# Kernel optimization log

Hardware: AMD Instinct MI355X
Metric: run time of the kernel (lower is better)

## Reference

```python
import jax, jax.numpy as jnp
import numpy as np

EPS = 1e-5
K = 3
N_TAP = K * K


def _bn(x, g, b, m, v):
    # eval-mode batchnorm over channel axis 1 of NCHW
    inv = g / jnp.sqrt(v + EPS)
    return x * inv[None, :, None, None] + (b - m * inv)[None, :, None, None]


def _silu(x):
    return x * jax.nn.sigmoid(x)


def _dcn(x, offset, mask, w, b, pad=1):
    """Modulated deformable conv (DCNv2), stride 1.
    x: [B,C,H,W], offset: [B,2n,H,W] ((dy,dx) per tap), mask: [B,n,H,W],
    w: [O,C,K,K], b: [O]."""
    B, C, H, W = x.shape
    O = w.shape[0]
    ky, kx = jnp.meshgrid(jnp.arange(K), jnp.arange(K), indexing='ij')
    ky = ky.reshape(N_TAP).astype(x.dtype)
    kx = kx.reshape(N_TAP).astype(x.dtype)
    off = offset.reshape(B, N_TAP, 2, H, W)
    base_y = jnp.arange(H, dtype=x.dtype)[None, None, :, None]
    base_x = jnp.arange(W, dtype=x.dtype)[None, None, None, :]
    # fractional sample positions [B,n,H,W]
    py = base_y - pad + ky[None, :, None, None] + off[:, :, 0]
    px = base_x - pad + kx[None, :, None, None] + off[:, :, 1]
    y0 = jnp.floor(py)
    x0 = jnp.floor(px)
    fy = py - y0
    fx = px - x0
    y0i = y0.astype(jnp.int32)
    x0i = x0.astype(jnp.int32)
    x_flat = x.reshape(B, C, 1, H * W)

    def corner(yi, xi, wgt):
        valid = (yi >= 0) & (yi < H) & (xi >= 0) & (xi < W)
        idx = (jnp.clip(yi, 0, H - 1) * W + jnp.clip(xi, 0, W - 1)).reshape(B, 1, N_TAP, H * W)
        v = jnp.take_along_axis(x_flat, idx, axis=-1)  # [B,C,n,HW]
        return v * (wgt * valid.astype(x.dtype)).reshape(B, 1, N_TAP, H * W)

    acc = corner(y0i, x0i, (1 - fy) * (1 - fx))
    acc = acc + corner(y0i, x0i + 1, (1 - fy) * fx)
    acc = acc + corner(y0i + 1, x0i, fy * (1 - fx))
    acc = acc + corner(y0i + 1, x0i + 1, fy * fx)
    val = acc.reshape(B, C, N_TAP, H, W) * mask[:, None]  # modulation
    out = jnp.einsum('bcnhw,ocn->bohw', val, w.reshape(O, C, N_TAP))
    return out + b[None, :, None, None]


def setup_inputs() -> dict:
    key = jax.random.key(0)
    ks = jax.random.split(key, 16)
    B, C1, H, W = 8, 256, 80, 80
    C2 = 256
    Ch = 128  # c_ = int(c2 * 0.5)
    d = {}
    d['x'] = jax.random.normal(ks[0], (B, C1, H, W), jnp.float32)
    # cv1: 1x1 conv (no bias) + BN
    d['cv1_w'] = jax.random.normal(ks[1], (Ch, C1), jnp.float32) * (1.0 / np.sqrt(C1))
    d['bn1_g'] = jax.random.uniform(ks[2], (Ch,), jnp.float32, 0.5, 1.5)
    d['bn1_b'] = jax.random.normal(ks[3], (Ch,), jnp.float32) * 0.1
    d['bn1_m'] = jax.random.normal(ks[4], (Ch,), jnp.float32) * 0.1
    d['bn1_v'] = jax.random.uniform(ks[5], (Ch,), jnp.float32, 0.5, 1.5)
    # offset/mask predictor 3x3 conv (small weights -> modest deformation)
    d['off_w'] = jax.random.normal(ks[6], (3 * N_TAP, Ch, K, K), jnp.float32) * 0.01
    d['off_b'] = jnp.zeros((3 * N_TAP,), jnp.float32)
    # dcn main weight/bias
    d['dcn_w'] = jax.random.normal(ks[7], (Ch, Ch, K, K), jnp.float32) * (1.0 / np.sqrt(Ch * N_TAP))
    d['dcn_b'] = jnp.zeros((Ch,), jnp.float32)
    d['bn2_g'] = jax.random.uniform(ks[8], (Ch,), jnp.float32, 0.5, 1.5)
    d['bn2_b'] = jax.random.normal(ks[9], (Ch,), jnp.float32) * 0.1
    d['bn2_m'] = jax.random.normal(ks[10], (Ch,), jnp.float32) * 0.1
    d['bn2_v'] = jax.random.uniform(ks[11], (Ch,), jnp.float32, 0.5, 1.5)
    # cv2: 1x1 conv (no bias) + BN
    d['cv2_w'] = jax.random.normal(ks[12], (C2, Ch), jnp.float32) * (1.0 / np.sqrt(Ch))
    d['bn3_g'] = jax.random.uniform(ks[13], (C2,), jnp.float32, 0.5, 1.5)
    d['bn3_b'] = jax.random.normal(ks[14], (C2,), jnp.float32) * 0.1
    d['bn3_m'] = jax.random.normal(ks[15], (C2,), jnp.float32) * 0.1
    d['bn3_v'] = jnp.ones((C2,), jnp.float32)
    return d


def reference(x, cv1_w, bn1_g, bn1_b, bn1_m, bn1_v,
              off_w, off_b, dcn_w, dcn_b, bn2_g, bn2_b, bn2_m, bn2_v,
              cv2_w, bn3_g, bn3_b, bn3_m, bn3_v):
    # cv1: 1x1 conv -> BN -> SiLU
    y = _silu(_bn(jnp.einsum('bchw,oc->bohw', x, cv1_w), bn1_g, bn1_b, bn1_m, bn1_v))
    # offset/mask predictor: 3x3 conv, pad 1
    raw = jax.lax.conv_general_dilated(
        y, off_w, window_strides=(1, 1), padding=((1, 1), (1, 1)),
        dimension_numbers=('NCHW', 'OIHW', 'NCHW')) + off_b[None, :, None, None]
    offset = raw[:, :2 * N_TAP]
    mask = jax.nn.sigmoid(raw[:, 2 * N_TAP:])
    # modulated deformable 3x3 conv -> BN -> SiLU
    y = _silu(_bn(_dcn(y, offset, mask, dcn_w, dcn_b), bn2_g, bn2_b, bn2_m, bn2_v))
    # cv2: 1x1 conv -> BN -> SiLU
    y = _silu(_bn(jnp.einsum('bchw,oc->bohw', y, cv2_w), bn3_g, bn3_b, bn3_m, bn3_v))
    return x + y  # shortcut (c1 == c2)
```

## Files before the change

kernel.cpp:

```cpp
#include <hip/hip_runtime.h>
#include <math.h>

#define HWSZ 6400
#define WIMG 80
#define HIMG 80
#define BEPS 1e-5f

typedef __attribute__((ext_vector_type(8))) short short8;
typedef __attribute__((ext_vector_type(4))) float f32x4;
typedef __attribute__((ext_vector_type(4))) unsigned u32x4;

__device__ __forceinline__ unsigned short f2b(float f) {
    unsigned u = __builtin_bit_cast(unsigned, f);
    u += 0x7fffu + ((u >> 16) & 1u);
    return (unsigned short)(u >> 16);
}
__device__ __forceinline__ float silu_f(float t) { return t / (1.f + __expf(-t)); }

#define BMFMA(a, b, c) __builtin_amdgcn_mfma_f32_16x16x32_bf16(a, b, c, 0, 0, 0)

__global__ __launch_bounds__(256) void k_prep(
    const float* __restrict__ cv1w, const float* __restrict__ g1, const float* __restrict__ b1,
    const float* __restrict__ m1, const float* __restrict__ v1,
    const float* __restrict__ offw, const float* __restrict__ offb,
    const float* __restrict__ dcnw, const float* __restrict__ dcnb,
    const float* __restrict__ g2, const float* __restrict__ b2,
    const float* __restrict__ m2, const float* __restrict__ v2,
    const float* __restrict__ cv2w, const float* __restrict__ g3, const float* __restrict__ b3,
    const float* __restrict__ m3, const float* __restrict__ v3,
    unsigned short* __restrict__ apk1, unsigned short* __restrict__ apko,
    unsigned short* __restrict__ apkd, unsigned short* __restrict__ apk2,
    float* __restrict__ bias1, float* __restrict__ biaso,
    float* __restrict__ bias2, float* __restrict__ bias3)
{
    int idx = blockIdx.x * 256 + threadIdx.x;
    if (idx < 32768) {
        int j = idx & 7, L = (idx >> 3) & 63, ks = (idx >> 9) & 7, mt = idx >> 12;
        int o = mt * 16 + (L & 15), k = ks * 32 + (L >> 4) * 8 + j;
        float inv = g1[o] * rsqrtf(v1[o] + BEPS);
        apk1[idx] = f2b(cv1w[o * 256 + k] * inv);
    } else if (idx < 69632) {
        int t = idx - 32768;
        int j = t & 7, L = (t >> 3) & 63;
        int mt = t / 18432, rem = t % 18432, ks = rem >> 9;
        int o = mt * 16 + (L & 15);
        int kp = ks * 32 + (L >> 4) * 8 + j;
        int n = kp >> 7, c = kp & 127;
        float wv = (o < 27) ? offw[(size_t)(o * 128 + c) * 9 + n] : 0.f;
        apko[((size_t)(ks * 2 + mt) * 64 + L) * 8 + j] = f2b(wv);
    } else if (idx < 217088) {
        int t = idx - 69632;
        int j = t & 7, L = (t >> 3) & 63;
        int mt = t / 18432, rem = t % 18432, ks = rem >> 9;
        int o = mt * 16 + (L & 15);
        int kp = ks * 32 + (L >> 4) * 8 + j;
        int n = kp >> 7, c = kp & 127;
        float inv = g2[o] * rsqrtf(v2[o] + BEPS);
        apkd[((size_t)(ks * 8 + mt) * 64 + L) * 8 + j] = f2b(dcnw[(size_t)(o * 128 + c) * 9 + n] * inv);
    } else if (idx < 249856) {
        int t = idx - 217088;
        int j = t & 7, L = (t >> 3) & 63, ks = (t >> 9) & 3, mt = t >> 11;
        int o = mt * 16 + (L & 15), k = ks * 32 + (L >> 4) * 8 + j;
        float inv = g3[o] * rsqrtf(v3[o] + BEPS);
        apk2[((size_t)(ks * 16 + mt) * 64 + L) * 8 + j] = f2b(cv2w[o * 128 + k] * inv);
    } else if (idx < 250395) {
        int t = idx - 249856;
        if (t < 128) { float inv = g1[t] * rsqrtf(v1[t] + BEPS); bias1[t] = b1[t] - m1[t] * inv; }
        else if (t < 155) { biaso[t - 128] = offb[t - 128]; }
        else if (t < 283) { int o = t - 155; float inv = g2[o] * rsqrtf(v2[o] + BEPS);
                            bias2[o] = dcnb[o] * inv + b2[o] - m2[o] * inv; }
        else { int o = t - 283; float inv = g3[o] * rsqrtf(v3[o] + BEPS); bias3[o] = b3[o] - m3[o] * inv; }
    }
}

__global__ __launch_bounds__(256) void k_cv1(
    const float* __restrict__ x, const unsigned short* __restrict__ apk1,
    const float* __restrict__ bias1, unsigned short* __restrict__ y1t)
{
    __shared__ __align__(16) unsigned short sB[20480];
    int blk = blockIdx.x;
    int b = blk / 100, pt = blk % 100;
    int p0 = pt * 64;
    int tid = threadIdx.x;
    int lane = tid & 63;
    int w = tid >> 6;
    {
        int px = lane, q = w;
        const float* xb = x + (size_t)b * 256 * HWSZ + p0 + px;
        for (int ks = 0; ks < 8; ++ks) {
            unsigned pk[4];
#pragma unroll
            for (int t = 0; t < 4; ++t) {
                float f0 = xb[(size_t)(ks * 32 + q * 8 + 2 * t) * HWSZ];
                float f1 = xb[(size_t)(ks * 32 + q * 8 + 2 * t + 1) * HWSZ];
                asm("v_cvt_pk_bf16_f32 %0, %1, %2" : "=v"(pk[t]) : "v"(f0), "v"(f1));
            }
            *(u32x4*)&sB[((ks * 4 + (px >> 4)) * 16 + (px & 15)) * 40 + q * 8] =
                (u32x4){pk[0], pk[1], pk[2], pk[3]};
        }
    }
    __syncthreads();
    int n16 = lane & 15, qd = lane >> 4;
    f32x4 acc[2][4];
#pragma unroll
    for (int mi = 0; mi < 2; ++mi)
#pragma unroll
        for (int nt = 0; nt < 4; ++nt) acc[mi][nt] = (f32x4){0.f, 0.f, 0.f, 0.f};
    for (int ks = 0; ks < 8; ++ks) {
        short8 bf[4];
#pragma unroll
        for (int nt = 0; nt < 4; ++nt)
            bf[nt] = *(const short8*)&sB[((ks * 4 + nt) * 16 + n16) * 40 + qd * 8];
        short8 a0 = *(const short8*)&apk1[(size_t)(((w * 2 + 0) * 8 + ks) * 64 + lane) * 8];
        short8 a1 = *(const short8*)&apk1[(size_t)(((w * 2 + 1) * 8 + ks) * 64 + lane) * 8];
#pragma unroll
        for (int nt = 0; nt < 4; ++nt) acc[0][nt] = BMFMA(a0, bf[nt], acc[0][nt]);
#pragma unroll
        for (int nt = 0; nt < 4; ++nt) acc[1][nt] = BMFMA(a1, bf[nt], acc[1][nt]);
    }
    __syncthreads();
#pragma unroll
    for (int mi = 0; mi < 2; ++mi)
#pragma unroll
        for (int nt = 0; nt < 4; ++nt)
#pragma unroll
            for (int r = 0; r < 4; ++r) {
                int o = w * 32 + mi * 16 + qd * 4 + r;
                float sv = silu_f(acc[mi][nt][r] + bias1[o]);
                sB[(nt * 16 + n16) * 136 + o] = f2b(sv);
            }
    __syncthreads();
    {
        int px = tid >> 2, qq = tid & 3;
        unsigned short* ytb = y1t + ((size_t)b * HWSZ + p0 + px) * 128;
#pragma unroll
        for (int seg = 0; seg < 4; ++seg) {
            short8 v = *(const short8*)&sB[px * 136 + qq * 32 + seg * 8];
            *(short8*)&ytb[qq * 32 + seg * 8] = v;
        }
    }
}

#define HY2 8
#define HX2 20
#define NH 160

#define ACC8(uu, cb)                                                                   \
    {                                                                                  \
        _Pragma("unroll") for (int t = 0; t < 4; ++t) {                                \
            unsigned uv = (uu)[t];                                                     \
            av[(cb) + 2 * t] = fmaf(wk, __builtin_bit_cast(float, uv << 16),           \
                                    av[(cb) + 2 * t]);                                 \
            av[(cb) + 2 * t + 1] = fmaf(wk, __builtin_bit_cast(float, uv & 0xffff0000u),\
                                        av[(cb) + 2 * t + 1]);                         \
        }                                                                              \
    }

#define LDA8(dst, ksv)                                                                 \
    _Pragma("unroll") for (int mt_ = 0; mt_ < 8; ++mt_)                                \
        dst[mt_] = *(const short8*)&apkd[((size_t)((ksv) * 8 + mt_) * 64 + lane) * 8];

#define MF8(afX, bfv)                                                                  \
    _Pragma("unroll") for (int mt_ = 0; mt_ < 8; ++mt_)                                \
        acc[mt_] = BMFMA(afX[mt_], bfv, acc[mt_]);

#define PACKBF(bfv, sv)                                                                \
    short8 bfv;                                                                        \
    {                                                                                  \
        unsigned pk0, pk1, pk2, pk3;                                                   \
        asm("v_cvt_pk_bf16_f32 %0, %1, %2" : "=v"(pk0) : "v"(av[(sv)*8+0]), "v"(av[(sv)*8+1])); \
        asm("v_cvt_pk_bf16_f32 %0, %1, %2" : "=v"(pk1) : "v"(av[(sv)*8+2]), "v"(av[(sv)*8+3])); \
        asm("v_cvt_pk_bf16_f32 %0, %1, %2" : "=v"(pk2) : "v"(av[(sv)*8+4]), "v"(av[(sv)*8+5])); \
        asm("v_cvt_pk_bf16_f32 %0, %1, %2" : "=v"(pk3) : "v"(av[(sv)*8+6]), "v"(av[(sv)*8+7])); \
        bfv = __builtin_bit_cast(short8, (u32x4){pk0, pk1, pk2, pk3});                 \
    }

__global__ __launch_bounds__(256, 3) void k_odc(
    const unsigned short* __restrict__ y1t,
    const unsigned short* __restrict__ apko, const float* __restrict__ biaso,
    const unsigned short* __restrict__ apkd, const float* __restrict__ bias2,
    const unsigned short* __restrict__ apk2, const float* __restrict__ bias3,
    const float* __restrict__ x, float* __restrict__ out)
{
    __shared__ __align__(16) unsigned short sH[NH * 128];
    __shared__ float sRaw[27 * 66];

    int blk = blockIdx.x;
    int b = blk / 100, pt = blk % 100;
    int h0 = (pt / 5) * 4, w0 = (pt % 5) * 16;
    int tid = threadIdx.x, lane = tid & 63, w = tid >> 6;
    int n16 = lane & 15, qd = lane >> 4;
    int pxl = w * 16 + n16;
    const unsigned short* yb = y1t + (size_t)b * HWSZ * 128;

    for (int i = tid; i < NH * 16; i += 256) {
        int r = i >> 4, u = i & 15;
        int ly = r / HX2, lx = r % HX2;
        int yy = min(max(h0 + ly - 2, 0), HIMG - 1);
        int xx = min(max(w0 + lx - 2, 0), WIMG - 1);
        *(u32x4*)&sH[r * 128 + ((u ^ (r & 7)) * 8)] =
            *(const u32x4*)&yb[(size_t)(yy * WIMG + xx) * 128 + u * 8];
    }
    __syncthreads();

    {
        f32x4 oa0 = (f32x4){0.f, 0.f, 0.f, 0.f};
        f32x4 oa1 = (f32x4){0.f, 0.f, 0.f, 0.f};
        for (int n = 0; n < 9; ++n) {
            int dh = n / 3 - 1, dw = n % 3 - 1;
            int hh = h0 + w + dh, ww = w0 + n16 + dw;
            bool valid = ((unsigned)hh < HIMG) && ((unsigned)ww < WIMG);
            int r = (w + 2 + dh) * HX2 + (n16 + 2 + dw);
            int xr = r & 7;
            const unsigned short* hb = &sH[r * 128];
#pragma unroll
            for (int s = 0; s < 4; ++s) {
                short8 bf = *(const short8*)&hb[((s * 4 + qd) ^ xr) * 8];
                if (!valid) bf = (short8){0, 0, 0, 0, 0, 0, 0, 0};
                int ks = n * 4 + s;
                short8 a0 = *(const short8*)&apko[((size_t)(ks * 2 + 0) * 64 + lane) * 8];
                short8 a1 = *(const short8*)&apko[((size_t)(ks * 2 + 1) * 64 + lane) * 8];
                oa0 = BMFMA(a0, bf, oa0);
                oa1 = BMFMA(a1, bf, oa1);
            }
        }
#pragma unroll
        for (int mi = 0; mi < 2; ++mi)
#pragma unroll
            for (int r4 = 0; r4 < 4; ++r4) {
                int o = mi * 16 + qd * 4 + r4;
                if (o < 27) {
                    float t = (mi ? oa1[r4] : oa0[r4]) + biaso[o];
                    if (o >= 18) t = 1.f / (1.f + __expf(-t));
                    sRaw[o * 66 + pxl] = t;
                }
            }
    }
    __syncthreads();

    f32x4 acc[8];
#pragma unroll
    for (int mt = 0; mt < 8; ++mt) acc[mt] = (f32x4){0.f, 0.f, 0.f, 0.f};
    int hI = h0 + w, wI = w0 + n16;

    for (int n = 0; n < 9; ++n) {
        float dy = sRaw[(2 * n) * 66 + pxl];
        float dx = sRaw[(2 * n + 1) * 66 + pxl];
        float mk = sRaw[(18 + n) * 66 + pxl];
        float py = (float)(hI - 1 + n / 3) + dy;
        float px = (float)(wI - 1 + n % 3) + dx;
        float y0f = floorf(py), x0f = floorf(px);
        float fy = py - y0f, fxv = px - x0f;
        int y0 = (int)y0f, x0 = (int)x0f;
        float wy0 = (1.f - fy) * mk, wy1 = fy * mk, fx1 = 1.f - fxv;

        int ks0 = n * 4;
        short8 afA[8], afB[8];
        LDA8(afA, ks0)

        float av[32];
#pragma unroll
        for (int j = 0; j < 32; ++j) av[j] = 0.f;
#pragma unroll
        for (int k = 0; k < 4; ++k) {
            int yy = y0 + (k >> 1), xx = x0 + (k & 1);
            bool vld = ((unsigned)yy < HIMG) && ((unsigned)xx < WIMG);
            float wk = ((k >> 1) ? wy1 : wy0) * ((k & 1) ? fxv : fx1);
            if (!vld) wk = 0.f;
            int yc = min(max(yy, 0), HIMG - 1);
            int xc = min(max(xx, 0), WIMG - 1);
            int ly = yc - h0 + 2, lx = xc - w0 + 2;
            if (((unsigned)ly < HY2) && ((unsigned)lx < HX2)) {
                int r = ly * HX2 + lx;
                const unsigned short* hb = &sH[r * 128];
                int xr = r & 7;
                u32x4 u0 = *(const u32x4*)&hb[((0 + qd) ^ xr) * 8];
                u32x4 u1 = *(const u32x4*)&hb[((4 + qd) ^ xr) * 8];
                u32x4 u2 = *(const u32x4*)&hb[((8 + qd) ^ xr) * 8];
                u32x4 u3 = *(const u32x4*)&hb[((12 + qd) ^ xr) * 8];
                ACC8(u0, 0) ACC8(u1, 8) ACC8(u2, 16) ACC8(u3, 24)
            } else if (wk != 0.f) {
                const unsigned short* src = &yb[(size_t)(yc * WIMG + xc) * 128 + qd * 8];
                u32x4 u0 = *(const u32x4*)src;
                u32x4 u1 = *(const u32x4*)(src + 32);
                u32x4 u2 = *(const u32x4*)(src + 64);
                u32x4 u3 = *(const u32x4*)(src + 96);
                ACC8(u0, 0) ACC8(u1, 8) ACC8(u2, 16) ACC8(u3, 24)
            }
        }
        LDA8(afB, ks0 + 1)
        { PACKBF(bf0, 0) MF8(afA, bf0) }
        LDA8(afA, ks0 + 2)
        { PACKBF(bf1, 1) MF8(afB, bf1) }
        LDA8(afB, ks0 + 3)
        { PACKBF(bf2, 2) MF8(afA, bf2) }
        { PACKBF(bf3, 3) MF8(afB, bf3) }
    }
    __syncthreads();

    unsigned short* sE = sH;
#pragma unroll
    for (int mt = 0; mt < 8; ++mt)
#pragma unroll
        for (int r4 = 0; r4 < 4; ++r4) {
            int o = mt * 16 + qd * 4 + r4;
            float sv = silu_f(acc[mt][r4] + bias2[o]);
            sE[pxl * 136 + o] = f2b(sv);
        }
    __syncthreads();

    f32x4 c2[16];
#pragma unroll
    for (int mt = 0; mt < 16; ++mt) c2[mt] = (f32x4){0.f, 0.f, 0.f, 0.f};
#pragma unroll
    for (int ks = 0; ks < 4; ++ks) {
        short8 bf = *(const short8*)&sE[pxl * 136 + ks * 32 + qd * 8];
        short8 cfA[8], cfB[8];
#pragma unroll
        for (int mt_ = 0; mt_ < 8; ++mt_)
            cfA[mt_] = *(const short8*)&apk2[((size_t)(ks * 16 + mt_) * 64 + lane) * 8];
#pragma unroll
        for (int mt_ = 0; mt_ < 8; ++mt_)
            cfB[mt_] = *(const short8*)&apk2[((size_t)(ks * 16 + 8 + mt_) * 64 + lane) * 8];
#pragma unroll
        for (int mt_ = 0; mt_ < 8; ++mt_) c2[mt_] = BMFMA(cfA[mt_], bf, c2[mt_]);
#pragma unroll
        for (int mt_ = 0; mt_ < 8; ++mt_) c2[8 + mt_] = BMFMA(cfB[mt_], bf, c2[8 + mt_]);
    }
    int p = (h0 + w) * WIMG + w0 + n16;
    const float* xb = x + (size_t)b * 256 * HWSZ;
    float* ob = out + (size_t)b * 256 * HWSZ;
#pragma unroll
    for (int mt = 0; mt < 16; ++mt)
#pragma unroll
        for (int r4 = 0; r4 < 4; ++r4) {
            int o = mt * 16 + qd * 4 + r4;
            size_t idx = (size_t)o * HWSZ + p;
            ob[idx] = xb[idx] + silu_f(c2[mt][r4] + bias3[o]);
        }
}

extern "C" void kernel_launch(void* const* d_in, const int* in_sizes, int n_in,
                              void* d_out, int out_size, void* d_ws, size_t ws_size,
                              hipStream_t stream) {
    const float* x     = (const float*)d_in[0];
    const float* cv1w  = (const float*)d_in[1];
    const float* bn1g  = (const float*)d_in[2];
    const float* bn1b  = (const float*)d_in[3];
    const float* bn1m  = (const float*)d_in[4];
    const float* bn1v  = (const float*)d_in[5];
    const float* offw  = (const float*)d_in[6];
    const float* offb  = (const float*)d_in[7];
    const float* dcnw  = (const float*)d_in[8];
    const float* dcnb  = (const float*)d_in[9];
    const float* bn2g  = (const float*)d_in[10];
    const float* bn2b  = (const float*)d_in[11];
    const float* bn2m  = (const float*)d_in[12];
    const float* bn2v  = (const float*)d_in[13];
    const float* cv2w  = (const float*)d_in[14];
    const float* bn3g  = (const float*)d_in[15];
    const float* bn3b  = (const float*)d_in[16];
    const float* bn3m  = (const float*)d_in[17];
    const float* bn3v  = (const float*)d_in[18];
    float* out = (float*)d_out;

    float* base = (float*)d_ws;
    unsigned short* y1t = (unsigned short*)base;
    unsigned short* apk1 = (unsigned short*)(base + 7936000);
    unsigned short* apko = (unsigned short*)(base + 7952384);
    unsigned short* apkd = (unsigned short*)(base + 7970816);
    unsigned short* apk2 = (unsigned short*)(base + 8044544);
    float* bias1 = base + 8060928;
    float* biaso = base + 8061056;
    float* bias2 = base + 8061088;
    float* bias3 = base + 8061216;

    k_prep<<<979, 256, 0, stream>>>(cv1w, bn1g, bn1b, bn1m, bn1v,
                                    offw, offb, dcnw, dcnb,
                                    bn2g, bn2b, bn2m, bn2v,
                                    cv2w, bn3g, bn3b, bn3m, bn3v,
                                    apk1, apko, apkd, apk2,
                                    bias1, biaso, bias2, bias3);
    k_cv1<<<800, 256, 0, stream>>>(x, apk1, bias1, y1t);
    k_odc<<<800, 256, 0, stream>>>(y1t, apko, biaso, apkd, bias2,
                                   apk2, bias3, x, out);
}
```

Before: 245.5 us.

## Stage packed weight slabs into double-buffered LDS via async global_load_lds

Weight fragments for the offset conv, the deformable conv and cv2 were each read from global memory straight into registers by every wave. They are now split into 53 slabs of 8 KB, copied into a two-buffer LDS area with global_load_lds one slab ahead, and read back from LDS for the MFMAs. Each slab step adds a block-wide barrier, launch bounds drop from 3 to 2 blocks per CU, and LDS use grows by 16 KB. The goal is to hide weight-load latency and cut duplicated global and L2 traffic across waves, at the cost of lower occupancy and many more barriers.

```diff
diff --git a/kernel.cpp b/kernel.cpp
--- a/kernel.cpp
+++ b/kernel.cpp
@@ -18,6 +18,12 @@
 __device__ __forceinline__ float silu_f(float t) { return t / (1.f + __expf(-t)); }
 
 #define BMFMA(a, b, c) __builtin_amdgcn_mfma_f32_16x16x32_bf16(a, b, c, 0, 0, 0)
+
+__device__ __forceinline__ void gload16(const unsigned short* g, unsigned short* l) {
+    __builtin_amdgcn_global_load_lds(
+        (const __attribute__((address_space(1))) unsigned int*)g,
+        (__attribute__((address_space(3))) unsigned int*)l, 16, 0, 0);
+}
 
 __global__ __launch_bounds__(256) void k_prep(
     const float* __restrict__ cv1w, const float* __restrict__ g1, const float* __restrict__ b1,
@@ -144,6 +150,7 @@
 #define HY2 8
 #define HX2 20
 #define NH 160
+#define NSLAB 53
 
 #define ACC8(uu, cb)                                                                   \
     {                                                                                  \
@@ -156,26 +163,22 @@
         }                                                                              \
     }
 
-#define LDA8(dst, ksv)                                                                 \
-    _Pragma("unroll") for (int mt_ = 0; mt_ < 8; ++mt_)                                \
-        dst[mt_] = *(const short8*)&apkd[((size_t)((ksv) * 8 + mt_) * 64 + lane) * 8];
-
-#define MF8(afX, bfv)                                                                  \
-    _Pragma("unroll") for (int mt_ = 0; mt_ < 8; ++mt_)                                \
-        acc[mt_] = BMFMA(afX[mt_], bfv, acc[mt_]);
-
-#define PACKBF(bfv, sv)                                                                \
-    short8 bfv;                                                                        \
+__device__ __forceinline__ const unsigned short* slab_src(
+    const unsigned short* apko, const unsigned short* apkd,
+    const unsigned short* apk2, int i) {
+    if (i < 9)  return apko + (size_t)i * 4096;
+    if (i < 45) return apkd + (size_t)(i - 9) * 4096;
+    return apk2 + (size_t)(i - 45) * 4096;
+}
+
+#define STAGE(i, bp)                                                                   \
     {                                                                                  \
-        unsigned pk0, pk1, pk2, pk3;                                                   \
-        asm("v_cvt_pk_bf16_f32 %0, %1, %2" : "=v"(pk0) : "v"(av[(sv)*8+0]), "v"(av[(sv)*8+1])); \
-        asm("v_cvt_pk_bf16_f32 %0, %1, %2" : "=v"(pk1) : "v"(av[(sv)*8+2]), "v"(av[(sv)*8+3])); \
-        asm("v_cvt_pk_bf16_f32 %0, %1, %2" : "=v"(pk2) : "v"(av[(sv)*8+4]), "v"(av[(sv)*8+5])); \
-        asm("v_cvt_pk_bf16_f32 %0, %1, %2" : "=v"(pk3) : "v"(av[(sv)*8+6]), "v"(av[(sv)*8+7])); \
-        bfv = __builtin_bit_cast(short8, (u32x4){pk0, pk1, pk2, pk3});                 \
-    }
-
-__global__ __launch_bounds__(256, 3) void k_odc(
+        const unsigned short* src_ = slab_src(apko, apkd, apk2, (i));                  \
+        gload16(src_ + ((w * 2 + 0) * 512 + lane * 8), &sAf[bp][(w * 2 + 0) * 512]);   \
+        gload16(src_ + ((w * 2 + 1) * 512 + lane * 8), &sAf[bp][(w * 2 + 1) * 512]);   \
+    }
+
+__global__ __launch_bounds__(256, 2) void k_odc(
     const unsigned short* __restrict__ y1t,
     const unsigned short* __restrict__ apko, const float* __restrict__ biaso,
     const unsigned short* __restrict__ apkd, const float* __restrict__ bias2,
@@ -184,6 +187,7 @@
 {
     __shared__ __align__(16) unsigned short sH[NH * 128];
     __shared__ float sRaw[27 * 66];
+    __shared__ __align__(16) unsigned short sAf[2][4096];
 
     int blk = blockIdx.x;
     int b = blk / 100, pt = blk % 100;
@@ -201,12 +205,15 @@
         *(u32x4*)&sH[r * 128 + ((u ^ (r & 7)) * 8)] =
             *(const u32x4*)&yb[(size_t)(yy * WIMG + xx) * 128 + u * 8];
     }
+    STAGE(0, 0)
     __syncthreads();
+    int bufp = 0;
 
     {
         f32x4 oa0 = (f32x4){0.f, 0.f, 0.f, 0.f};
         f32x4 oa1 = (f32x4){0.f, 0.f, 0.f, 0.f};
         for (int n = 0; n < 9; ++n) {
+            STAGE(n + 1, bufp ^ 1)
             int dh = n / 3 - 1, dw = n % 3 - 1;
             int hh = h0 + w + dh, ww = w0 + n16 + dw;
             bool valid = ((unsigned)hh < HIMG) && ((unsigned)ww < WIMG);
@@ -217,26 +224,28 @@
             for (int s = 0; s < 4; ++s) {
                 short8 bf = *(const short8*)&hb[((s * 4 + qd) ^ xr) * 8];
                 if (!valid) bf = (short8){0, 0, 0, 0, 0, 0, 0, 0};
-                int ks = n * 4 + s;
-                short8 a0 = *(const short8*)&apko[((size_t)(ks * 2 + 0) * 64 + lane) * 8];
-                short8 a1 = *(const short8*)&apko[((size_t)(ks * 2 + 1) * 64 + lane) * 8];
+                short8 a0 = *(const short8*)&sAf[bufp][(s * 2 + 0) * 512 + lane * 8];
+                short8 a1 = *(const short8*)&sAf[bufp][(s * 2 + 1) * 512 + lane * 8];
                 oa0 = BMFMA(a0, bf, oa0);
                 oa1 = BMFMA(a1, bf, oa1);
             }
-        }
-#pragma unroll
-        for (int mi = 0; mi < 2; ++mi)
-#pragma unroll
-            for (int r4 = 0; r4 < 4; ++r4) {
-                int o = mi * 16 + qd * 4 + r4;
-                if (o < 27) {
-                    float t = (mi ? oa1[r4] : oa0[r4]) + biaso[o];
-                    if (o >= 18) t = 1.f / (1.f + __expf(-t));
-                    sRaw[o * 66 + pxl] = t;
-                }
-            }
-    }
-    __syncthreads();
+            if (n == 8) {
+#pragma unroll
+                for (int mi = 0; mi < 2; ++mi)
+#pragma unroll
+                    for (int r4 = 0; r4 < 4; ++r4) {
+                        int o = mi * 16 + qd * 4 + r4;
+                        if (o < 27) {
+                            float t = (mi ? oa1[r4] : oa0[r4]) + biaso[o];
+                            if (o >= 18) t = 1.f / (1.f + __expf(-t));
+                            sRaw[o * 66 + pxl] = t;
+                        }
+                    }
+            }
+            __syncthreads();
+            bufp ^= 1;
+        }
+    }
 
     f32x4 acc[8];
 #pragma unroll
@@ -244,88 +253,95 @@
     int hI = h0 + w, wI = w0 + n16;
 
     for (int n = 0; n < 9; ++n) {
-        float dy = sRaw[(2 * n) * 66 + pxl];
-        float dx = sRaw[(2 * n + 1) * 66 + pxl];
-        float mk = sRaw[(18 + n) * 66 + pxl];
-        float py = (float)(hI - 1 + n / 3) + dy;
-        float px = (float)(wI - 1 + n % 3) + dx;
-        float y0f = floorf(py), x0f = floorf(px);
-        float fy = py - y0f, fxv = px - x0f;
-        int y0 = (int)y0f, x0 = (int)x0f;
-        float wy0 = (1.f - fy) * mk, wy1 = fy * mk, fx1 = 1.f - fxv;
-
-        int ks0 = n * 4;
-        short8 afA[8], afB[8];
-        LDA8(afA, ks0)
-
         float av[32];
 #pragma unroll
-        for (int j = 0; j < 32; ++j) av[j] = 0.f;
-#pragma unroll
-        for (int k = 0; k < 4; ++k) {
-            int yy = y0 + (k >> 1), xx = x0 + (k & 1);
-            bool vld = ((unsigned)yy < HIMG) && ((unsigned)xx < WIMG);
-            float wk = ((k >> 1) ? wy1 : wy0) * ((k & 1) ? fxv : fx1);
-            if (!vld) wk = 0.f;
-            int yc = min(max(yy, 0), HIMG - 1);
-            int xc = min(max(xx, 0), WIMG - 1);
-            int ly = yc - h0 + 2, lx = xc - w0 + 2;
-            if (((unsigned)ly < HY2) && ((unsigned)lx < HX2)) {
-                int r = ly * HX2 + lx;
-                const unsigned short* hb = &sH[r * 128];
-                int xr = r & 7;
-                u32x4 u0 = *(const u32x4*)&hb[((0 + qd) ^ xr) * 8];
-                u32x4 u1 = *(const u32x4*)&hb[((4 + qd) ^ xr) * 8];
-                u32x4 u2 = *(const u32x4*)&hb[((8 + qd) ^ xr) * 8];
-                u32x4 u3 = *(const u32x4*)&hb[((12 + qd) ^ xr) * 8];
-                ACC8(u0, 0) ACC8(u1, 8) ACC8(u2, 16) ACC8(u3, 24)
-            } else if (wk != 0.f) {
-                const unsigned short* src = &yb[(size_t)(yc * WIMG + xc) * 128 + qd * 8];
-                u32x4 u0 = *(const u32x4*)src;
-                u32x4 u1 = *(const u32x4*)(src + 32);
-                u32x4 u2 = *(const u32x4*)(src + 64);
-                u32x4 u3 = *(const u32x4*)(src + 96);
-                ACC8(u0, 0) ACC8(u1, 8) ACC8(u2, 16) ACC8(u3, 24)
-            }
-        }
-        LDA8(afB, ks0 + 1)
-        { PACKBF(bf0, 0) MF8(afA, bf0) }
-        LDA8(afA, ks0 + 2)
-        { PACKBF(bf1, 1) MF8(afB, bf1) }
-        LDA8(afB, ks0 + 3)
-        { PACKBF(bf2, 2) MF8(afA, bf2) }
-        { PACKBF(bf3, 3) MF8(afB, bf3) }
-    }
-    __syncthreads();
-
-    unsigned short* sE = sH;
-#pragma unroll
-    for (int mt = 0; mt < 8; ++mt)
-#pragma unroll
-        for (int r4 = 0; r4 < 4; ++r4) {
-            int o = mt * 16 + qd * 4 + r4;
-            float sv = silu_f(acc[mt][r4] + bias2[o]);
-            sE[pxl * 136 + o] = f2b(sv);
-        }
-    __syncthreads();
-
+        for (int s = 0; s < 4; ++s) {
+            int slab = 9 + n * 4 + s;
+            if (slab + 1 < NSLAB) STAGE(slab + 1, bufp ^ 1)
+            if (s == 0) {
+                float dy = sRaw[(2 * n) * 66 + pxl];
+                float dx = sRaw[(2 * n + 1) * 66 + pxl];
+                float mk = sRaw[(18 + n) * 66 + pxl];
+                float py = (float)(hI - 1 + n / 3) + dy;
+                float px = (float)(wI - 1 + n % 3) + dx;
+                float y0f = floorf(py), x0f = floorf(px);
+                float fy = py - y0f, fxv = px - x0f;
+                int y0 = (int)y0f, x0 = (int)x0f;
+                float wy0 = (1.f - fy) * mk, wy1 = fy * mk, fx1 = 1.f - fxv;
+#pragma unroll
+                for (int j = 0; j < 32; ++j) av[j] = 0.f;
+#pragma unroll
+                for (int k = 0; k < 4; ++k) {
+                    int yy = y0 + (k >> 1), xx = x0 + (k & 1);
+                    bool vld = ((unsigned)yy < HIMG) && ((unsigned)xx < WIMG);
+                    float wk = ((k >> 1) ? wy1 : wy0) * ((k & 1) ? fxv : fx1);
+                    if (!vld) wk = 0.f;
+                    int yc = min(max(yy, 0), HIMG - 1);
+                    int xc = min(max(xx, 0), WIMG - 1);
+                    int ly = yc - h0 + 2, lx = xc - w0 + 2;
+                    if (((unsigned)ly < HY2) && ((unsigned)lx < HX2)) {
+                        int r = ly * HX2 + lx;
+                        const unsigned short* hb = &sH[r * 128];
+                        int xr = r & 7;
+                        u32x4 u0 = *(const u32x4*)&hb[((0 + qd) ^ xr) * 8];
+                        u32x4 u1 = *(const u32x4*)&hb[((4 + qd) ^ xr) * 8];
+                        u32x4 u2 = *(const u32x4*)&hb[((8 + qd) ^ xr) * 8];
+                        u32x4 u3 = *(const u32x4*)&hb[((12 + qd) ^ xr) * 8];
+                        ACC8(u0, 0) ACC8(u1, 8) ACC8(u2, 16) ACC8(u3, 24)
+                    } else if (wk != 0.f) {
+                        const unsigned short* src = &yb[(size_t)(yc * WIMG + xc) * 128 + qd * 8];
+                        u32x4 u0 = *(const u32x4*)src;
+                        u32x4 u1 = *(const u32x4*)(src + 32);
+                        u32x4 u2 = *(const u32x4*)(src + 64);
+                        u32x4 u3 = *(const u32x4*)(src + 96);
+                        ACC8(u0, 0) ACC8(u1, 8) ACC8(u2, 16) ACC8(u3, 24)
+                    }
+                }
+            }
+            unsigned pk0, pk1, pk2, pk3;
+            asm("v_cvt_pk_bf16_f32 %0, %1, %2" : "=v"(pk0) : "v"(av[s * 8 + 0]), "v"(av[s * 8 + 1]));
+            asm("v_cvt_pk_bf16_f32 %0, %1, %2" : "=v"(pk1) : "v"(av[s * 8 + 2]), "v"(av[s * 8 + 3]));
+            asm("v_cvt_pk_bf16_f32 %0, %1, %2" : "=v"(pk2) : "v"(av[s * 8 + 4]), "v"(av[s * 8 + 5]));
+            asm("v_cvt_pk_bf16_f32 %0, %1, %2" : "=v"(pk3) : "v"(av[s * 8 + 6]), "v"(av[s * 8 + 7]));
+            short8 bfv = __builtin_bit_cast(short8, (u32x4){pk0, pk1, pk2, pk3});
+#pragma unroll
+            for (int mt = 0; mt < 8; ++mt) {
+                short8 af = *(const short8*)&sAf[bufp][mt * 512 + lane * 8];
+                acc[mt] = BMFMA(af, bfv, acc[mt]);
+            }
+            if (n == 8 && s == 3) {
+                unsigned short* sE = sH;
+#pragma unroll
+                for (int mt = 0; mt < 8; ++mt)
+#pragma unroll
+                    for (int r4 = 0; r4 < 4; ++r4) {
+                        int o = mt * 16 + qd * 4 + r4;
+                        float sv = silu_f(acc[mt][r4] + bias2[o]);
+                        sE[pxl * 136 + o] = f2b(sv);
+                    }
+            }
+            __syncthreads();
+            bufp ^= 1;
+        }
+    }
+
+    const unsigned short* sE = sH;
     f32x4 c2[16];
 #pragma unroll
     for (int mt = 0; mt < 16; ++mt) c2[mt] = (f32x4){0.f, 0.f, 0.f, 0.f};
 #pragma unroll
-    for (int ks = 0; ks < 4; ++ks) {
+    for (int h2 = 0; h2 < 8; ++h2) {
+        int slab = 45 + h2;
+        if (slab + 1 < NSLAB) STAGE(slab + 1, bufp ^ 1)
+        int ks = h2 >> 1, half = h2 & 1;
         short8 bf = *(const short8*)&sE[pxl * 136 + ks * 32 + qd * 8];
-        short8 cfA[8], cfB[8];
-#pragma unroll
-        for (int mt_ = 0; mt_ < 8; ++mt_)
-            cfA[mt_] = *(const short8*)&apk2[((size_t)(ks * 16 + mt_) * 64 + lane) * 8];
-#pragma unroll
-        for (int mt_ = 0; mt_ < 8; ++mt_)
-            cfB[mt_] = *(const short8*)&apk2[((size_t)(ks * 16 + 8 + mt_) * 64 + lane) * 8];
-#pragma unroll
-        for (int mt_ = 0; mt_ < 8; ++mt_) c2[mt_] = BMFMA(cfA[mt_], bf, c2[mt_]);
-#pragma unroll
-        for (int mt_ = 0; mt_ < 8; ++mt_) c2[8 + mt_] = BMFMA(cfB[mt_], bf, c2[8 + mt_]);
+#pragma unroll
+        for (int mt = 0; mt < 8; ++mt) {
+            short8 af = *(const short8*)&sAf[bufp][mt * 512 + lane * 8];
+            c2[half * 8 + mt] = BMFMA(af, bf, c2[half * 8 + mt]);
+        }
+        __syncthreads();
+        bufp ^= 1;
     }
     int p = (h0 + w) * WIMG + w0 + n16;
     const float* xb = x + (size_t)b * 256 * HWSZ;
```

Measured after the change: 235.1 us. 4.2% less time.
